# Kernel optimization log

Measured on AMD Instinct MI355X. Metric: run time of the kernel, lower is better.

The kernel has to match this reference:

```python
import jax, jax.numpy as jnp
import numpy as np

DIM = 1024
DEPTH = 3
BATCH = 8
SEQ = DIM  # module requires seq_len == dim for the residual add to broadcast


def setup_inputs() -> dict:
    key = jax.random.key(0)
    k1, k2, k3, k4 = jax.random.split(key, 4)
    x = jax.random.normal(k1, (BATCH, SEQ, DIM), dtype=jnp.float32)
    # torch.nn.Linear(dim, 3*dim): weight [3*dim, dim], bias [3*dim]
    Wqkv = jax.random.normal(k2, (3 * DIM, DIM), dtype=jnp.float32) * (1.0 / np.sqrt(DIM))
    bqkv = jax.random.normal(k3, (3 * DIM,), dtype=jnp.float32) * 0.01
    # self.w: Parameter of shape [depth, dim, dim], init randn
    w = jax.random.normal(k4, (DEPTH, DIM, DIM), dtype=jnp.float32)
    return {"x": x, "Wqkv": Wqkv, "bqkv": bqkv, "w": w}


def reference(x, Wqkv, bqkv, w):
    # qkv projection then chunk into q, k, v along last dim
    qkv = x @ Wqkv.T + bqkv                      # [B, S, 3*dim]
    q, k, v = jnp.split(qkv, 3, axis=-1)         # each [B, S, dim]
    scale = 1.0 / (q.shape[-1] ** 0.5)
    # sum over depth of (q @ w[i]) @ k^T, accumulated onto v
    # einsum contracts d (dim), e (dim), and sums over n (depth) in one pass
    scores = jnp.einsum('bsd,nde,bte->bst', q, w, k)  # [B, S, S]; requires S == dim
    return v + scores * scale
```

## Files before the change

### kernel.cpp

```cpp
#include <hip/hip_runtime.h>
#include <hip/hip_bf16.h>
#include <stdint.h>

typedef __bf16 bf16_t;
typedef __bf16 bf16x8 __attribute__((ext_vector_type(8)));
typedef __bf16 bf16x4 __attribute__((ext_vector_type(4)));
typedef float  f32x4  __attribute__((ext_vector_type(4)));

#define DIM   1024
#define BATCH 8
#define NTOK  (BATCH * DIM)
#define SCALE 0.03125f

__global__ void k_cvt(const float* __restrict__ in, bf16_t* __restrict__ out, int n4) {
    int i = blockIdx.x * blockDim.x + threadIdx.x;
    if (i < n4) {
        const float4 v = reinterpret_cast<const float4*>(in)[i];
        bf16x4 o;
        o.x = (bf16_t)v.x; o.y = (bf16_t)v.y; o.z = (bf16_t)v.z; o.w = (bf16_t)v.w;
        reinterpret_cast<bf16x4*>(out)[i] = o;
    }
}

__global__ void k_weff(const float* __restrict__ w, bf16_t* __restrict__ wt) {
    __shared__ float tile[32][33];
    const int tx = threadIdx.x & 31;
    const int ty = threadIdx.x >> 5;
    const int d0 = blockIdx.x * 32;
    const int e0 = blockIdx.y * 32;
#pragma unroll
    for (int r = 0; r < 4; ++r) {
        const int d = d0 + r * 8 + ty;
        const int e = e0 + tx;
        tile[r * 8 + ty][tx] =
            w[d * 1024 + e] + w[1048576 + d * 1024 + e] + w[2097152 + d * 1024 + e];
    }
    __syncthreads();
#pragma unroll
    for (int r = 0; r < 4; ++r) {
        const int e = e0 + r * 8 + ty;
        const int d = d0 + tx;
        wt[e * 1024 + d] = (bf16_t)tile[tx][r * 8 + ty];
    }
}

__global__ void k_trans(const float* __restrict__ in, bf16_t* __restrict__ out) {
    __shared__ float tile[32][33];
    const int tx = threadIdx.x & 31;
    const int ty = threadIdx.x >> 5;
    const int e0 = blockIdx.x * 32;
    const int d0 = blockIdx.y * 32;
#pragma unroll
    for (int r = 0; r < 4; ++r)
        tile[r * 8 + ty][tx] = in[(long)(e0 + r * 8 + ty) * 1024 + d0 + tx];
    __syncthreads();
#pragma unroll
    for (int r = 0; r < 4; ++r)
        out[(long)(d0 + r * 8 + ty) * 1024 + e0 + tx] = (bf16_t)tile[tx][r * 8 + ty];
}

__global__ void k_bqw(const float* __restrict__ bq, const bf16_t* __restrict__ wtb,
                      float* __restrict__ bqw) {
    const int wave = threadIdx.x >> 6, lane = threadIdx.x & 63;
    const int n = blockIdx.x * 4 + wave;
    const bf16_t* row = wtb + (long)n * 1024;
    float s = 0.f;
#pragma unroll
    for (int c = 0; c < 2; ++c) {
        const int d0 = (lane + c * 64) * 8;
        const bf16x8 v = *reinterpret_cast<const bf16x8*>(row + d0);
#pragma unroll
        for (int e = 0; e < 8; ++e) s += bq[d0 + e] * (float)v[e];
    }
#pragma unroll
    for (int off = 32; off; off >>= 1) s += __shfl_down(s, off);
    if (lane == 0) bqw[n] = s;
}

__global__ __launch_bounds__(256)
void k_sk(const bf16_t* __restrict__ A, const bf16_t* __restrict__ B,
          float* __restrict__ oAt)
{
    __shared__ __align__(16) bf16_t As[128 * 32];
    __shared__ __align__(16) bf16_t Bs[128 * 32];

    const int tid  = threadIdx.x;
    const int wave = tid >> 6;
    const int lane = tid & 63;
    const int wr = wave >> 1, wc = wave & 1;
    const int lhi = lane >> 4, llo = lane & 15;

    const int bm = blockIdx.x * 128;
    const int bn = blockIdx.y * 128;
    const int kb = blockIdx.z * 256;

    f32x4 acc[4][4];
    const f32x4 fz = {0.f, 0.f, 0.f, 0.f};
#pragma unroll
    for (int i = 0; i < 4; ++i)
#pragma unroll
        for (int j = 0; j < 4; ++j) acc[i][j] = fz;

    for (int k0 = 0; k0 < 256; k0 += 32) {
#pragma unroll
        for (int i = 0; i < 2; ++i) {
            const int c  = wave * 128 + i * 64 + lane;
            const int r  = c >> 2;
            const int cc = (c & 3) << 3;
            const long ga = (long)(bm + r) * 1024 + kb + k0 + cc;
            const long gb = (long)(bn + r) * 1024 + kb + k0 + cc;
            const int lbase = (wave * 128 + i * 64) << 3;
            __builtin_amdgcn_global_load_lds(
                (const __attribute__((address_space(1))) uint32_t*)(A + ga),
                (__attribute__((address_space(3))) uint32_t*)(&As[lbase]), 16, 0, 0);
            __builtin_amdgcn_global_load_lds(
                (const __attribute__((address_space(1))) uint32_t*)(B + gb),
                (__attribute__((address_space(3))) uint32_t*)(&Bs[lbase]), 16, 0, 0);
        }
        __syncthreads();

        bf16x8 af[4], bfr[4];
#pragma unroll
        for (int mi = 0; mi < 4; ++mi)
            af[mi] = *reinterpret_cast<const bf16x8*>(&As[(wr * 64 + mi * 16 + llo) * 32 + lhi * 8]);
#pragma unroll
        for (int ni = 0; ni < 4; ++ni)
            bfr[ni] = *reinterpret_cast<const bf16x8*>(&Bs[(wc * 64 + ni * 16 + llo) * 32 + lhi * 8]);
#pragma unroll
        for (int mi = 0; mi < 4; ++mi)
#pragma unroll
            for (int ni = 0; ni < 4; ++ni)
                acc[mi][ni] = __builtin_amdgcn_mfma_f32_16x16x32_bf16(af[mi], bfr[ni], acc[mi][ni], 0, 0, 0);
        __syncthreads();
    }

#pragma unroll
    for (int mi = 0; mi < 4; ++mi) {
        const int r0 = bm + wr * 64 + mi * 16 + lhi * 4;
#pragma unroll
        for (int ni = 0; ni < 4; ++ni) {
            const int cg = bn + wc * 64 + ni * 16 + llo;
            const f32x4 v = acc[mi][ni];
#pragma unroll
            for (int j = 0; j < 4; ++j)
                atomicAdd(&oAt[(long)(r0 + j) * 1024 + cg], v[j]);
        }
    }
}

template<int BN_, int MODE>
__global__ __launch_bounds__(512, 2)
void k_db(const bf16_t* __restrict__ A, const bf16_t* __restrict__ Bp,
          const float* __restrict__ bqw, const float* __restrict__ bqkv,
          bf16_t* __restrict__ oQW, bf16_t* __restrict__ oK, float* __restrict__ oF)
{
    constexpr int NF   = BN_ / 64;
    constexpr int LB   = BN_ / 64;
    constexpr int LPT  = 2 + LB;
    constexpr int SLOT = (128 + BN_) * 128;
    constexpr int NTT  = 16;
    __shared__ __align__(16) unsigned char slds[2 * SLOT];

    const int tid  = threadIdx.x;
    const int wave = tid >> 6, lane = tid & 63;
    const int wm = wave >> 2, wn = wave & 3;
    const int llo = lane & 15, lhi = lane >> 4;

    int bm, bn; long zz = 0;
    if (MODE == 1) {
        bm = blockIdx.x * 128; bn = blockIdx.y * BN_;
    } else {
        const int nw = ((int)blockIdx.x & 7) * 64 + ((int)blockIdx.x >> 3);
        zz = (long)(nw >> 6) << 20;
        const int r = nw & 63;
        bm = (r >> 3) * 128; bn = (r & 7) * 128;
    }

    const bf16_t* sp[LPT]; int dst[LPT];
#pragma unroll
    for (int j = 0; j < 2; ++j) {
        const int C = j * 512 + tid;
        const int r = C >> 3, u = (C & 7) ^ (r & 7);
        sp[j] = A + zz + (long)(bm + r) * 1024 + (u << 3);
        dst[j] = C << 4;
    }
#pragma unroll
    for (int j = 0; j < LB; ++j) {
        const int C = j * 512 + tid;
        const int r = C >> 3, u = (C & 7) ^ (r & 7);
        sp[2 + j] = Bp + zz + (long)(bn + r) * 1024 + (u << 3);
        dst[2 + j] = 16384 + (C << 4);
    }

    auto stage = [&](int tt) {
        unsigned char* s = &slds[(tt & 1) * SLOT];
        const long ko = (long)tt << 6;
#pragma unroll
        for (int j = 0; j < LPT; ++j)
            __builtin_amdgcn_global_load_lds(
                (const __attribute__((address_space(1))) uint32_t*)(sp[j] + ko),
                (__attribute__((address_space(3))) uint32_t*)(s + dst[j]), 16, 0, 0);
    };

    f32x4 acc[4][NF];
    const f32x4 fz = {0.f, 0.f, 0.f, 0.f};
#pragma unroll
    for (int i = 0; i < 4; ++i)
#pragma unroll
        for (int j = 0; j < NF; ++j) acc[i][j] = fz;

    stage(0);

    for (int t = 0; t < NTT; ++t) {
        if (t + 1 < NTT) {
            stage(t + 1);
            asm volatile("s_waitcnt vmcnt(%0)" :: "i"(LPT) : "memory");
        } else {
            asm volatile("s_waitcnt vmcnt(0)" ::: "memory");
        }
        __builtin_amdgcn_s_barrier();

        const unsigned char* sb = &slds[(t & 1) * SLOT];
#pragma unroll
        for (int ks = 0; ks < 2; ++ks) {
            bf16x8 af[4], bfv[NF];
#pragma unroll
            for (int mi = 0; mi < 4; ++mi) {
                const int r = wm * 64 + mi * 16 + llo;
                af[mi] = *reinterpret_cast<const bf16x8*>(
                    sb + r * 128 + ((((ks << 2) | lhi) ^ (r & 7)) << 4));
            }
#pragma unroll
            for (int ni = 0; ni < NF; ++ni) {
                const int r = wn * (NF * 16) + ni * 16 + llo;
                bfv[ni] = *reinterpret_cast<const bf16x8*>(
                    sb + 16384 + r * 128 + ((((ks << 2) | lhi) ^ (r & 7)) << 4));
            }
            __builtin_amdgcn_s_setprio(1);
#pragma unroll
            for (int mi = 0; mi < 4; ++mi)
#pragma unroll
                for (int ni = 0; ni < NF; ++ni)
                    acc[mi][ni] = __builtin_amdgcn_mfma_f32_16x16x32_bf16(
                        af[mi], bfv[ni], acc[mi][ni], 0, 0, 0);
            __builtin_amdgcn_s_setprio(0);
        }
        asm volatile("s_waitcnt lgkmcnt(0)" ::: "memory");
        __builtin_amdgcn_s_barrier();
    }

#pragma unroll
    for (int mi = 0; mi < 4; ++mi) {
        const long r0 = bm + wm * 64 + mi * 16 + lhi * 4;
#pragma unroll
        for (int ni = 0; ni < NF; ++ni) {
            const int cg = bn + wn * (NF * 16) + ni * 16 + llo;
            const f32x4 v = acc[mi][ni];
            if (MODE == 1) {
                const int sec = cg >> 10;
                const int c1  = cg & 1023;
                const float bb = (sec == 0) ? bqw[cg] : bqkv[cg];
#pragma unroll
                for (int j = 0; j < 4; ++j) {
                    const long idx = (r0 + j) * 1024 + c1;
                    const float val = v[j] + bb;
                    if (sec == 0)      oQW[idx] = (bf16_t)val;
                    else if (sec == 1) oK[idx] = (bf16_t)val;
                    else               oF[idx] = val;
                }
            } else {
#pragma unroll
                for (int j = 0; j < 4; ++j) {
                    const long idx = zz + (r0 + j) * 1024 + cg;
                    oF[idx] = oF[idx] + SCALE * v[j];
                }
            }
        }
    }
}

extern "C" void kernel_launch(void* const* d_in, const int* in_sizes, int n_in,
                              void* d_out, int out_size, void* d_ws, size_t ws_size,
                              hipStream_t stream) {
    const float* x    = (const float*)d_in[0];
    const float* Wqkv = (const float*)d_in[1];
    const float* bqkv = (const float*)d_in[2];
    const float* w    = (const float*)d_in[3];
    float* out = (float*)d_out;

    char* ws = (char*)d_ws;
    bf16_t* xb   = (bf16_t*)(ws);
    bf16_t* wbig = (bf16_t*)(ws + (16l << 20));
    float*  bqw  = (float*) (ws + (22l << 20));
    bf16_t* kb   = (bf16_t*)(ws + (22l << 20) + 65536);
    bf16_t* qwb  = (bf16_t*)(ws + (38l << 20) + 65536);
    bf16_t* wtb  = qwb;
    bf16_t* wqt  = qwb + 1048576;
    float*  bp32 = (float*)(qwb + 2097152);
    if (ws_size < (size_t)(54l << 20) + 65536) return;

    k_cvt  <<<8192, 256, 0, stream>>>(x, xb, 2097152);
    k_cvt  <<<2048, 256, 0, stream>>>(Wqkv + 1048576, wbig + 1048576, 524288);
    k_weff <<<dim3(32, 32), 256, 0, stream>>>(w, wtb);
    k_trans<<<dim3(32, 32), 256, 0, stream>>>(Wqkv, wqt);
    k_bqw  <<<256, 256, 0, stream>>>(bqkv, wtb, bqw);

    hipMemsetAsync(bp32, 0, 4194304, stream);
    k_sk <<<dim3(8, 8, 4), 256, 0, stream>>>(wtb, wqt, bp32);
    k_cvt<<<1024, 256, 0, stream>>>(bp32, wbig, 262144);

    k_db<192, 1><<<dim3(64, 16), 512, 0, stream>>>(xb, wbig, bqw, bqkv, qwb, kb, out);

    k_db<128, 2><<<dim3(512), 512, 0, stream>>>(qwb, kb, nullptr, nullptr,
                                                nullptr, nullptr, out);
}
```

Baseline: 125.6 us.

## Enlarge GEMM tiles to 256 rows with fine-grained interleaved load/MFMA pipeline

Both main GEMM kernels are rewritten to use 256-row M tiles (8 MFMA row fragments per wave) and a four-phase inner loop. Each phase issues part of the next stage's global-to-LDS loads between LDS reads and MFMA bursts, with partial vmcnt waits, instead of loading a whole stage then computing. Block-to-XCD mapping is also reworked so blocks sharing A/B rows land on the same XCD. The goals are more reuse per loaded byte and better overlap of memory with compute. The cost is more accumulator registers, more LDS per block, and fewer blocks (256 for the second GEMM), which can hurt occupancy and tail balance.

```diff
diff --git a/kernel.cpp b/kernel.cpp
--- a/kernel.cpp
+++ b/kernel.cpp
@@ -148,16 +148,22 @@
     }
 }
 
-template<int BN_, int MODE>
+#define GLOAD(SRC, DST) __builtin_amdgcn_global_load_lds( \
+    (const __attribute__((address_space(1))) uint32_t*)(SRC), \
+    (__attribute__((address_space(3))) uint32_t*)(DST), 16, 0, 0)
+
+template<int MODE>
 __global__ __launch_bounds__(512, 2)
-void k_db(const bf16_t* __restrict__ A, const bf16_t* __restrict__ Bp,
-          const float* __restrict__ bqw, const float* __restrict__ bqkv,
-          bf16_t* __restrict__ oQW, bf16_t* __restrict__ oK, float* __restrict__ oF)
+void k8(const bf16_t* __restrict__ A, const bf16_t* __restrict__ Bp,
+        const float* __restrict__ bias_q, const float* __restrict__ bias_kv,
+        bf16_t* __restrict__ oQW, bf16_t* __restrict__ oK,
+        float* __restrict__ oV, float* __restrict__ oF)
 {
-    constexpr int NF   = BN_ / 64;
-    constexpr int LB   = BN_ / 64;
-    constexpr int LPT  = 2 + LB;
-    constexpr int SLOT = (128 + BN_) * 128;
+    constexpr int NF   = (MODE == 1) ? 3 : 2;
+    constexpr int BN   = NF * 64;
+    constexpr int NB   = BN / 64;
+    constexpr int NP   = 4 + NB;
+    constexpr int SLOT = 32768 + BN * 128;
     constexpr int NTT  = 16;
     __shared__ __align__(16) unsigned char slds[2 * SLOT];
 
@@ -166,118 +172,173 @@
     const int wm = wave >> 2, wn = wave & 3;
     const int llo = lane & 15, lhi = lane >> 4;
 
-    int bm, bn; long zz = 0;
+    int bmA, bnB, bnOut;
     if (MODE == 1) {
-        bm = blockIdx.x * 128; bn = blockIdx.y * BN_;
+        const int xcd = (int)blockIdx.x & 7, idx = (int)blockIdx.x >> 3;
+        bmA  = (xcd * 4 + (idx >> 4)) * 256;
+        bnB  = (idx & 15) * 192;
+        bnOut = bnB;
     } else {
-        const int nw = ((int)blockIdx.x & 7) * 64 + ((int)blockIdx.x >> 3);
-        zz = (long)(nw >> 6) << 20;
-        const int r = nw & 63;
-        bm = (r >> 3) * 128; bn = (r & 7) * 128;
-    }
-
-    const bf16_t* sp[LPT]; int dst[LPT];
-#pragma unroll
-    for (int j = 0; j < 2; ++j) {
-        const int C = j * 512 + tid;
-        const int r = C >> 3, u = (C & 7) ^ (r & 7);
-        sp[j] = A + zz + (long)(bm + r) * 1024 + (u << 3);
-        dst[j] = C << 4;
-    }
-#pragma unroll
-    for (int j = 0; j < LB; ++j) {
-        const int C = j * 512 + tid;
-        const int r = C >> 3, u = (C & 7) ^ (r & 7);
-        sp[2 + j] = Bp + zz + (long)(bn + r) * 1024 + (u << 3);
-        dst[2 + j] = 16384 + (C << 4);
-    }
-
-    auto stage = [&](int tt) {
-        unsigned char* s = &slds[(tt & 1) * SLOT];
-        const long ko = (long)tt << 6;
-#pragma unroll
-        for (int j = 0; j < LPT; ++j)
-            __builtin_amdgcn_global_load_lds(
-                (const __attribute__((address_space(1))) uint32_t*)(sp[j] + ko),
-                (__attribute__((address_space(3))) uint32_t*)(s + dst[j]), 16, 0, 0);
-    };
-
-    f32x4 acc[4][NF];
+        const int xcd = (int)blockIdx.x & 7, idx = (int)blockIdx.x >> 3;
+        bmA  = xcd * 1024 + (idx >> 3) * 256;
+        bnOut = (idx & 7) * 128;
+        bnB  = xcd * 1024 + bnOut;
+    }
+
+    const int prow = tid >> 3;
+    const int uch  = (tid & 7) ^ (prow & 7);
+    const bf16_t* sp[NP]; int dst[NP];
+#pragma unroll
+    for (int j = 0; j < 4; ++j) {
+        const int row = j * 64 + prow;
+        sp[j]  = A + (long)(bmA + row) * 1024 + uch * 8;
+        dst[j] = row * 128 + (tid & 7) * 16;
+    }
+#pragma unroll
+    for (int j = 0; j < NB; ++j) {
+        const int row = j * 64 + prow;
+        sp[4 + j]  = Bp + (long)(bnB + row) * 1024 + uch * 8;
+        dst[4 + j] = 32768 + row * 128 + (tid & 7) * 16;
+    }
+
+#define STG(TT, J) GLOAD(sp[J] + (long)(TT) * 64, slds + ((TT) & 1) * SLOT + dst[J])
+
+    f32x4 acc[8][NF];
     const f32x4 fz = {0.f, 0.f, 0.f, 0.f};
 #pragma unroll
-    for (int i = 0; i < 4; ++i)
+    for (int i = 0; i < 8; ++i)
 #pragma unroll
         for (int j = 0; j < NF; ++j) acc[i][j] = fz;
 
-    stage(0);
-
-    for (int t = 0; t < NTT; ++t) {
-        if (t + 1 < NTT) {
-            stage(t + 1);
-            asm volatile("s_waitcnt vmcnt(%0)" :: "i"(LPT) : "memory");
-        } else {
-            asm volatile("s_waitcnt vmcnt(0)" ::: "memory");
-        }
-        __builtin_amdgcn_s_barrier();
-
-        const unsigned char* sb = &slds[(t & 1) * SLOT];
-#pragma unroll
-        for (int ks = 0; ks < 2; ++ks) {
-            bf16x8 af[4], bfv[NF];
-#pragma unroll
-            for (int mi = 0; mi < 4; ++mi) {
-                const int r = wm * 64 + mi * 16 + llo;
-                af[mi] = *reinterpret_cast<const bf16x8*>(
-                    sb + r * 128 + ((((ks << 2) | lhi) ^ (r & 7)) << 4));
-            }
-#pragma unroll
-            for (int ni = 0; ni < NF; ++ni) {
-                const int r = wn * (NF * 16) + ni * 16 + llo;
-                bfv[ni] = *reinterpret_cast<const bf16x8*>(
-                    sb + 16384 + r * 128 + ((((ks << 2) | lhi) ^ (r & 7)) << 4));
-            }
-            __builtin_amdgcn_s_setprio(1);
-#pragma unroll
-            for (int mi = 0; mi < 4; ++mi)
-#pragma unroll
-                for (int ni = 0; ni < NF; ++ni)
-                    acc[mi][ni] = __builtin_amdgcn_mfma_f32_16x16x32_bf16(
-                        af[mi], bfv[ni], acc[mi][ni], 0, 0, 0);
-            __builtin_amdgcn_s_setprio(0);
-        }
+#pragma unroll
+    for (int j = 0; j < NP; ++j) STG(0, j);
+    STG(1, 4); STG(1, 5);
+    asm volatile("s_waitcnt vmcnt(2)" ::: "memory");
+    __builtin_amdgcn_s_barrier();
+
+    for (int u = 0; u < NTT; ++u) {
+        const unsigned char* rb = slds + (u & 1) * SLOT;
+        bf16x8 af[4], bfv[NF];
+
+#pragma unroll
+        for (int mi = 0; mi < 4; ++mi) {
+            const int r = wm * 128 + mi * 16 + llo;
+            af[mi] = *reinterpret_cast<const bf16x8*>(rb + r * 128 + ((lhi ^ (r & 7)) << 4));
+        }
+#pragma unroll
+        for (int ni = 0; ni < NF; ++ni) {
+            const int r = wn * (NF * 16) + ni * 16 + llo;
+            bfv[ni] = *reinterpret_cast<const bf16x8*>(rb + 32768 + r * 128 + ((lhi ^ (r & 7)) << 4));
+        }
+        if (u + 1 < NTT) {
+            if (MODE == 1) STG(u + 1, 6);
+            else           STG(u + 1, 2);
+            STG(u + 1, 0);
+        }
+        __builtin_amdgcn_s_barrier();
         asm volatile("s_waitcnt lgkmcnt(0)" ::: "memory");
-        __builtin_amdgcn_s_barrier();
-    }
-
-#pragma unroll
-    for (int mi = 0; mi < 4; ++mi) {
-        const long r0 = bm + wm * 64 + mi * 16 + lhi * 4;
+        __builtin_amdgcn_s_setprio(1);
+#pragma unroll
+        for (int mi = 0; mi < 4; ++mi)
+#pragma unroll
+            for (int ni = 0; ni < NF; ++ni)
+                acc[mi][ni] = __builtin_amdgcn_mfma_f32_16x16x32_bf16(af[mi], bfv[ni], acc[mi][ni], 0, 0, 0);
+        __builtin_amdgcn_s_setprio(0);
+        asm volatile("s_waitcnt vmcnt(4)" ::: "memory");
+        __builtin_amdgcn_s_barrier();
+
+#pragma unroll
+        for (int mi = 0; mi < 4; ++mi) {
+            const int r = wm * 128 + (mi + 4) * 16 + llo;
+            af[mi] = *reinterpret_cast<const bf16x8*>(rb + r * 128 + ((lhi ^ (r & 7)) << 4));
+        }
+        if (u + 1 < NTT) {
+            if (MODE == 1) { STG(u + 1, 2); STG(u + 1, 1); }
+            else           STG(u + 1, 1);
+        }
+        __builtin_amdgcn_s_barrier();
+        asm volatile("s_waitcnt lgkmcnt(0)" ::: "memory");
+        __builtin_amdgcn_s_setprio(1);
+#pragma unroll
+        for (int mi = 0; mi < 4; ++mi)
+#pragma unroll
+            for (int ni = 0; ni < NF; ++ni)
+                acc[mi + 4][ni] = __builtin_amdgcn_mfma_f32_16x16x32_bf16(af[mi], bfv[ni], acc[mi + 4][ni], 0, 0, 0);
+        __builtin_amdgcn_s_setprio(0);
+        __builtin_amdgcn_s_barrier();
+
+#pragma unroll
+        for (int mi = 0; mi < 4; ++mi) {
+            const int r = wm * 128 + mi * 16 + llo;
+            af[mi] = *reinterpret_cast<const bf16x8*>(rb + r * 128 + (((4 | lhi) ^ (r & 7)) << 4));
+        }
 #pragma unroll
         for (int ni = 0; ni < NF; ++ni) {
-            const int cg = bn + wn * (NF * 16) + ni * 16 + llo;
+            const int r = wn * (NF * 16) + ni * 16 + llo;
+            bfv[ni] = *reinterpret_cast<const bf16x8*>(rb + 32768 + r * 128 + (((4 | lhi) ^ (r & 7)) << 4));
+        }
+        if (u + 1 < NTT) STG(u + 1, 3);
+        __builtin_amdgcn_s_barrier();
+        asm volatile("s_waitcnt lgkmcnt(0)" ::: "memory");
+        __builtin_amdgcn_s_setprio(1);
+#pragma unroll
+        for (int mi = 0; mi < 4; ++mi)
+#pragma unroll
+            for (int ni = 0; ni < NF; ++ni)
+                acc[mi][ni] = __builtin_amdgcn_mfma_f32_16x16x32_bf16(af[mi], bfv[ni], acc[mi][ni], 0, 0, 0);
+        __builtin_amdgcn_s_setprio(0);
+        __builtin_amdgcn_s_barrier();
+
+#pragma unroll
+        for (int mi = 0; mi < 4; ++mi) {
+            const int r = wm * 128 + (mi + 4) * 16 + llo;
+            af[mi] = *reinterpret_cast<const bf16x8*>(rb + r * 128 + (((4 | lhi) ^ (r & 7)) << 4));
+        }
+        if (u + 2 < NTT) { STG(u + 2, 4); STG(u + 2, 5); }
+        __builtin_amdgcn_s_barrier();
+        asm volatile("s_waitcnt lgkmcnt(0)" ::: "memory");
+        __builtin_amdgcn_s_setprio(1);
+#pragma unroll
+        for (int mi = 0; mi < 4; ++mi)
+#pragma unroll
+            for (int ni = 0; ni < NF; ++ni)
+                acc[mi + 4][ni] = __builtin_amdgcn_mfma_f32_16x16x32_bf16(af[mi], bfv[ni], acc[mi + 4][ni], 0, 0, 0);
+        __builtin_amdgcn_s_setprio(0);
+        asm volatile("s_waitcnt vmcnt(4)" ::: "memory");
+        __builtin_amdgcn_s_barrier();
+    }
+
+#pragma unroll
+    for (int mi = 0; mi < 8; ++mi) {
+        const long r0 = bmA + wm * 128 + mi * 16 + lhi * 4;
+#pragma unroll
+        for (int ni = 0; ni < NF; ++ni) {
+            const int cg = bnOut + wn * (NF * 16) + ni * 16 + llo;
             const f32x4 v = acc[mi][ni];
             if (MODE == 1) {
                 const int sec = cg >> 10;
                 const int c1  = cg & 1023;
-                const float bb = (sec == 0) ? bqw[cg] : bqkv[cg];
+                const float bb = (sec == 0) ? bias_q[cg] : bias_kv[cg];
 #pragma unroll
                 for (int j = 0; j < 4; ++j) {
                     const long idx = (r0 + j) * 1024 + c1;
                     const float val = v[j] + bb;
                     if (sec == 0)      oQW[idx] = (bf16_t)val;
                     else if (sec == 1) oK[idx] = (bf16_t)val;
-                    else               oF[idx] = val;
+                    else               oV[idx] = val;
                 }
             } else {
 #pragma unroll
                 for (int j = 0; j < 4; ++j) {
-                    const long idx = zz + (r0 + j) * 1024 + cg;
+                    const long idx = (r0 + j) * 1024 + cg;
                     oF[idx] = oF[idx] + SCALE * v[j];
                 }
             }
         }
     }
 }
+#undef STG
+#undef GLOAD
 
 extern "C" void kernel_launch(void* const* d_in, const int* in_sizes, int n_in,
                               void* d_out, int out_size, void* d_ws, size_t ws_size,
@@ -309,8 +370,8 @@
     k_sk <<<dim3(8, 8, 4), 256, 0, stream>>>(wtb, wqt, bp32);
     k_cvt<<<1024, 256, 0, stream>>>(bp32, wbig, 262144);
 
-    k_db<192, 1><<<dim3(64, 16), 512, 0, stream>>>(xb, wbig, bqw, bqkv, qwb, kb, out);
-
-    k_db<128, 2><<<dim3(512), 512, 0, stream>>>(qwb, kb, nullptr, nullptr,
-                                                nullptr, nullptr, out);
-}
+    k8<1><<<512, 512, 0, stream>>>(xb, wbig, bqw, bqkv, qwb, kb, out, nullptr);
+
+    k8<2><<<256, 512, 0, stream>>>(qwb, kb, nullptr, nullptr,
+                                   nullptr, nullptr, nullptr, out);
+}
```

New measurement: 140.6 us. +11.9%, slower.
